# Kernel optimization log

Measured on AMD Instinct MI355X. Metric: run time of the kernel, lower is better.

The kernel has to match this reference:

```python
import jax, jax.numpy as jnp
import numpy as np

REPR_IN = (16, 16, 8)
REPR_OUT = (32, 16, 8)
NUM_BASIS = 16
MAX_RADIUS = 2.0
GAMMA = 16.0  # radial basis sharpness

def _dim(repr_):
    return sum(m * (2 * l + 1) for l, m in enumerate(repr_))

DIM_IN = _dim(REPR_IN)          # 104
SIZE_OUT = _dim(REPR_OUT)       # 120
NUM_GATES = sum(REPR_OUT[1:])   # 24
DIM_OUT = SIZE_OUT + NUM_GATES  # 144 (conv emits gates too)


def setup_inputs() -> dict:
    key = jax.random.key(0)
    k1, k2, k3, k4 = jax.random.split(key, 4)
    B, N, M = 4, 1024, 1024
    features = jax.random.normal(k1, (B, DIM_IN, M), jnp.float32)
    difference_matrix = jax.random.normal(k2, (B, N, M, 3), jnp.float32)
    relative_mask = jax.random.uniform(k3, (B, N, M), jnp.float32)
    W = jax.random.normal(k4, (NUM_BASIS, DIM_OUT, DIM_IN), jnp.float32) / np.sqrt(NUM_BASIS * DIM_IN)
    return {"features": features, "difference_matrix": difference_matrix,
            "relative_mask": relative_mask, "W": W}


def _radial_basis(diff):
    # diff: [B, N, M, 3] -> phi: [B, N, M, K]
    r = jnp.sqrt(jnp.sum(diff * diff, axis=-1) + 1e-12)
    centers = jnp.linspace(0.0, MAX_RADIUS, NUM_BASIS, dtype=diff.dtype)
    return jnp.exp(-GAMMA * jnp.square(r[..., None] - centers))


def reference(features, difference_matrix, relative_mask, W):
    # SE3PointConvolution: per-pair kernel K[b,n,m] = sum_k phi_k(|r_nm|) W[k]
    # masked by relative_mask; out[b,o,n] = sum_m K[b,n,m,o,i] feat[b,i,m].
    # Fused so the [B,N,M,144,104] kernel is never materialized.
    phi = _radial_basis(difference_matrix) * relative_mask[..., None]  # [B,N,M,K]
    tmp = jnp.einsum('bnmk,bim->bnki', phi, features)                  # [B,N,K,DIM_IN]
    y = jnp.einsum('bnki,koi->bon', tmp, W)                            # [B,DIM_OUT,N]

    B, _, N = y.shape
    # scalar (l=0) activation, bias=False
    outs = [jax.nn.relu(y[:, :REPR_OUT[0]])]
    # gates: last NUM_GATES channels, sigmoid
    g = jax.nn.sigmoid(y[:, SIZE_OUT:])
    begin_y, begin_g = REPR_OUT[0], 0
    for l, mul in enumerate(REPR_OUT):
        if l == 0 or mul == 0:
            continue
        d = 2 * l + 1
        fy = y[:, begin_y:begin_y + mul * d].reshape(B, mul, d, N)
        fg = g[:, begin_g:begin_g + mul].reshape(B, mul, 1, N)
        outs.append((fy * fg).reshape(B, mul * d, N))
        begin_y += mul * d
        begin_g += mul
    return jnp.concatenate(outs, axis=1)  # [B, SIZE_OUT, N]
```

## Files before the change

kernel.cpp:

```cpp
#include <hip/hip_runtime.h>


typedef __attribute__((ext_vector_type(4))) float f32x4;
typedef __attribute__((ext_vector_type(8))) short s16x8;

#define DI 104
#define DO 144
#define MT 64
#define PST 72
#define TTST 1688
#define YST 9

#define W_ELEMS 239616
#define F_ELEMS 425984

#define OFF_PHI0 0
#define OFF_PHI1 18432
#define OFF_FEAT0 36864
#define OFF_FEAT1 52992
#define OFF_Y 69120
#define SMEM_TOTAL (69120 + 144*9*4)

__device__ __forceinline__ float fexp2(float x) {
#if __has_builtin(__builtin_amdgcn_exp2f)
    return __builtin_amdgcn_exp2f(x);
#else
    return exp2f(x);
#endif
}
__device__ __forceinline__ float flog2(float x) {
#if __has_builtin(__builtin_amdgcn_logf)
    return __builtin_amdgcn_logf(x);
#else
    return log2f(x);
#endif
}
__device__ __forceinline__ float fsqrt_(float x) {
#if __has_builtin(__builtin_amdgcn_sqrtf)
    return __builtin_amdgcn_sqrtf(x);
#else
    return sqrtf(x);
#endif
}
__device__ __forceinline__ float frcp_(float x) {
#if __has_builtin(__builtin_amdgcn_rcpf)
    return __builtin_amdgcn_rcpf(x);
#else
    return 1.0f / x;
#endif
}
__device__ __forceinline__ unsigned int pkbf(float lo, float hi) {
    unsigned int a = __builtin_bit_cast(unsigned int, lo) + 0x8000u;
    unsigned int b = __builtin_bit_cast(unsigned int, hi) + 0x8000u;
    return __builtin_amdgcn_perm(b, a, 0x07060302u);
}
__device__ __forceinline__ unsigned short f2b(float f) {
    return (unsigned short)((__builtin_bit_cast(unsigned int, f) + 0x8000u) >> 16);
}

__global__ __launch_bounds__(256, 8)
void cvt_kernel(const float* __restrict__ feat_g, const float* __restrict__ W_g,
                unsigned short* __restrict__ ws)
{
    int gid = blockIdx.x * 256 + threadIdx.x;
    const float* src;
    unsigned short* dst;
    if (gid < W_ELEMS/8) {
        src = W_g + gid*8;  dst = ws + gid*8;
    } else {
        int g2 = gid - W_ELEMS/8;
        src = feat_g + g2*8; dst = ws + W_ELEMS + g2*8;
    }
    f32x4 a = *(const f32x4*)src;
    f32x4 b = *(const f32x4*)(src + 4);
    unsigned int o[4] = { pkbf(a[0],a[1]), pkbf(a[2],a[3]), pkbf(b[0],b[1]), pkbf(b[2],b[3]) };
    *(f32x4*)dst = *(f32x4*)o;
}

__global__ __launch_bounds__(512, 4)
void pgb_kernel(const unsigned short* __restrict__ ws,
                const float* __restrict__ diff_g,
                const float* __restrict__ mask_g,
                float* __restrict__ out_g)
{
    const unsigned short* Wbf    = ws;
    const unsigned short* featbf = ws + W_ELEMS;

    __shared__ __align__(16) unsigned char smem[SMEM_TOTAL];
    unsigned short* Tt   = (unsigned short*)(smem);
    float*          ylds = (float*)(smem + OFF_Y);

    const int t    = threadIdx.x;
    const int b    = blockIdx.x >> 7;
    const int n0   = (blockIdx.x & 127) << 3;
    const int wave = t >> 6;
    const int lane = t & 63;
    const int l15  = lane & 15;
    const int q    = lane >> 4;
    const int wr   = wave >> 1;
    const int ct0  = (wave & 1) << 2;

    {
        unsigned int* p0 = (unsigned int*)(smem + OFF_FEAT0 + DI*PST*2);
        unsigned int* p1 = (unsigned int*)(smem + OFF_FEAT1 + DI*PST*2);
        if (t < 288) { p0[t] = 0u; p1[t] = 0u; }
    }

    f32x4 acc[2][4];
#pragma unroll
    for (int rr = 0; rr < 2; ++rr)
#pragma unroll
        for (int cc = 0; cc < 4; ++cc)
            acc[rr][cc] = (f32x4){0.f, 0.f, 0.f, 0.f};

    const int pn = t >> 6;
    const int kh = (t >> 5) & 1;
    const int pm = (t & 31) << 1;
    const float CEXP = -23.083120654223414f;
    const float A1   = 6.155498841126244f;
    const float V2   = -0.8207331788168325f;
    const float K0OFF = kh ? 1.0666666666666667f : 0.f;
    const float S0B   = kh ? -6.976232019943076f : -0.41036658940841624f;
    const size_t dmrow = (size_t)((b << 10) + n0 + pn) << 10;

    const int fi0 = t >> 3, part0 = (t & 7) << 3;
    const int fi1 = 64 + (t >> 3);
    const size_t fbase = (size_t)b * DI << 10;

    float dx0, dy0, dz0, dx1, dy1, dz1, mk0, mk1;
    s16x8 fr0, fr1;
    {
        const float* dp = diff_g + (dmrow + pm)*3;
        dx0=dp[0]; dy0=dp[1]; dz0=dp[2]; dx1=dp[3]; dy1=dp[4]; dz1=dp[5];
        const float* mp = mask_g + dmrow + pm;
        mk0=mp[0]; mk1=mp[1];
        fr0 = *(const s16x8*)(featbf + fbase + ((size_t)fi0 << 10) + part0);
        if (t < 320)
            fr1 = *(const s16x8*)(featbf + fbase + ((size_t)fi1 << 10) + part0);
    }

    for (int s = 0; s < 16; ++s) {
        const int ms = s * MT;
        unsigned short* phibuf  = (unsigned short*)(smem + ((s & 1) ? OFF_PHI1 : OFF_PHI0));
        unsigned short* featbuf = (unsigned short*)(smem + ((s & 1) ? OFF_FEAT1 : OFF_FEAT0));
        float nx0=0, ny0=0, nz0=0, nx1=0, ny1=0, nz1=0, nm0=0, nm1=0;
        s16x8 nf0, nf1;
        if (s < 15) {
            const float* dp = diff_g + (dmrow + ms + MT + pm)*3;
            nx0=dp[0]; ny0=dp[1]; nz0=dp[2]; nx1=dp[3]; ny1=dp[4]; nz1=dp[5];
            const float* mp = mask_g + dmrow + ms + MT + pm;
            nm0=mp[0]; nm1=mp[1];
            nf0 = *(const s16x8*)(featbf + fbase + ((size_t)fi0 << 10) + ms + MT + part0);
            if (t < 320)
                nf1 = *(const s16x8*)(featbf + fbase + ((size_t)fi1 << 10) + ms + MT + part0);
        }
        {
            float r0 = fsqrt_(fmaf(dx0,dx0, fmaf(dy0,dy0, fmaf(dz0,dz0, 1e-12f))));
            float r1 = fsqrt_(fmaf(dx1,dx1, fmaf(dy1,dy1, fmaf(dz1,dz1, 1e-12f))));
            float t0 = r0 - K0OFF, t1 = r1 - K0OFF;
            float E0 = fmaf(CEXP*t0, t0, flog2(mk0));
            float E1 = fmaf(CEXP*t1, t1, flog2(mk1));
            float s0 = fmaf(A1, r0, S0B);
            float s1 = fmaf(A1, r1, S0B);
            unsigned short* pw = phibuf + (pn*16 + kh*8)*PST + pm;
#pragma unroll
            for (int j = 0; j < 8; ++j) {
                float p0 = fexp2(E0);
                float p1 = fexp2(E1);
                *(unsigned int*)(pw + j*PST) = pkbf(p0, p1);
                E0 += s0; s0 += V2;
                E1 += s1; s1 += V2;
            }
        }
        *(s16x8*)(featbuf + fi0*PST + part0) = fr0;
        if (t < 320)
            *(s16x8*)(featbuf + fi1*PST + part0) = fr1;
        __syncthreads();
#pragma unroll
        for (int kk = 0; kk < 2; ++kk) {
            const int mo = kk*32 + q*8;
            s16x8 a0 = *(const s16x8*)(phibuf + ((2*wr    )*16 + l15)*PST + mo);
            s16x8 a1 = *(const s16x8*)(phibuf + ((2*wr + 1)*16 + l15)*PST + mo);
#pragma unroll
            for (int cc = 0; cc < 4; ++cc) {
                if (ct0 + cc < 7) {
                    s16x8 bf = *(const s16x8*)(featbuf + ((ct0+cc)*16 + l15)*PST + mo);
                    acc[0][cc] = __builtin_amdgcn_mfma_f32_16x16x32_bf16(a0, bf, acc[0][cc], 0, 0, 0);
                    acc[1][cc] = __builtin_amdgcn_mfma_f32_16x16x32_bf16(a1, bf, acc[1][cc], 0, 0, 0);
                }
            }
        }
        dx0=nx0; dy0=ny0; dz0=nz0; dx1=nx1; dy1=ny1; dz1=nz1; mk0=nm0; mk1=nm1;
        fr0 = nf0; if (t < 320) fr1 = nf1;
    }

    __syncthreads();

#pragma unroll
    for (int rr = 0; rr < 2; ++rr) {
        int nloc = 2*wr + rr;
#pragma unroll
        for (int cc = 0; cc < 4; ++cc) {
            int i = (ct0+cc)*16 + l15;
            if (ct0 + cc < 7 && i < DI) {
#pragma unroll
                for (int r = 0; r < 4; ++r)
                    Tt[nloc*TTST + (q*4+r)*DI + i] = f2b(acc[rr][cc][r]);
            }
        }
    }
    __syncthreads();

    f32x4 y0 = (f32x4){0.f,0.f,0.f,0.f}, y1 = (f32x4){0.f,0.f,0.f,0.f};
    const int o0 = wave*16 + l15;
    const int o1 = 128 + l15;
#pragma unroll 4
    for (int s3 = 0; s3 < 52; ++s3) {
        int a = s3*4 + q;
        int k = a / 13;
        int i = (a - k*13) << 3;
        s16x8 bf = *(const s16x8*)(Tt + (l15 & 7)*TTST + s3*32 + q*8);
        s16x8 af = *(const s16x8*)(Wbf + (size_t)(k*DO + o0)*DI + i);
        y0 = __builtin_amdgcn_mfma_f32_16x16x32_bf16(af, bf, y0, 0, 0, 0);
        if (wave == 0) {
            s16x8 ag = *(const s16x8*)(Wbf + (size_t)(k*DO + o1)*DI + i);
            y1 = __builtin_amdgcn_mfma_f32_16x16x32_bf16(ag, bf, y1, 0, 0, 0);
        }
    }
    if (l15 < 8) {
#pragma unroll
        for (int r = 0; r < 4; ++r)
            ylds[(wave*16 + q*4 + r)*YST + l15] = y0[r];
        if (wave == 0) {
#pragma unroll
            for (int r = 0; r < 4; ++r)
                ylds[(128 + q*4 + r)*YST + l15] = y1[r];
        }
    }
    __syncthreads();

    const float L2E = 1.4426950408889634f;
    for (int idx = t; idx < 120*8; idx += 512) {
        int o = idx >> 3, nn = idx & 7;
        float y = ylds[o*YST + nn];
        float v;
        if (o < 32) {
            v = fmaxf(y, 0.f);
        } else if (o < 80) {
            float g = ylds[(120 + (o-32)/3)*YST + nn];
            v = y * frcp_(1.f + fexp2(-g*L2E));
        } else {
            float g = ylds[(136 + (o-80)/5)*YST + nn];
            v = y * frcp_(1.f + fexp2(-g*L2E));
        }
        out_g[((size_t)(b*120 + o) << 10) + n0 + nn] = v;
    }
}

extern "C" void kernel_launch(void* const* d_in, const int* in_sizes, int n_in,
                              void* d_out, int out_size, void* d_ws, size_t ws_size,
                              hipStream_t stream) {
    const float* feat = (const float*)d_in[0];
    const float* diff = (const float*)d_in[1];
    const float* mask = (const float*)d_in[2];
    const float* W    = (const float*)d_in[3];
    float* out = (float*)d_out;
    unsigned short* ws = (unsigned short*)d_ws;
    (void)in_sizes; (void)n_in; (void)out_size; (void)ws_size;
    cvt_kernel<<<dim3((W_ELEMS + F_ELEMS)/8/256), dim3(256), 0, stream>>>(feat, W, ws);
    pgb_kernel<<<dim3(512), dim3(512), 0, stream>>>(ws, diff, mask, out);
}
```

Baseline: 142.4 us.

## Swizzle LDS tiles instead of padding and move next-tile prefetch after barrier

The padded LDS row stride (72) for the phi and feature tiles is replaced by an unpadded 64-element stride with an XOR swizzle on 8-element chunks, applied on both the write and the MFMA operand read paths. This shrinks shared memory use while still avoiding bank conflicts. Global loads for the next tile now go after the barrier straight into the live registers, which drops the separate next-tile registers and can lower register pressure. The risk is that load latency is less hidden behind the phi computation.

```diff
diff --git a/kernel.cpp b/kernel.cpp
--- a/kernel.cpp
+++ b/kernel.cpp
@@ -7,7 +7,6 @@
 #define DI 104
 #define DO 144
 #define MT 64
-#define PST 72
 #define TTST 1688
 #define YST 9
 
@@ -15,11 +14,11 @@
 #define F_ELEMS 425984
 
 #define OFF_PHI0 0
-#define OFF_PHI1 18432
-#define OFF_FEAT0 36864
-#define OFF_FEAT1 52992
-#define OFF_Y 69120
-#define SMEM_TOTAL (69120 + 144*9*4)
+#define OFF_PHI1 16384
+#define OFF_FEAT0 32768
+#define OFF_FEAT1 47104
+#define OFF_Y 61440
+#define SMEM_TOTAL (61440 + 144*9*4)
 
 __device__ __forceinline__ float fexp2(float x) {
 #if __has_builtin(__builtin_amdgcn_exp2f)
@@ -99,11 +98,11 @@
     const int q    = lane >> 4;
     const int wr   = wave >> 1;
     const int ct0  = (wave & 1) << 2;
-
-    {
-        unsigned int* p0 = (unsigned int*)(smem + OFF_FEAT0 + DI*PST*2);
-        unsigned int* p1 = (unsigned int*)(smem + OFF_FEAT1 + DI*PST*2);
-        if (t < 288) { p0[t] = 0u; p1[t] = 0u; }
+    const int sw   = l15 & 7;
+
+    if (t < 256) {
+        ((unsigned int*)(smem + OFF_FEAT0 + DI*128))[t] = 0u;
+        ((unsigned int*)(smem + OFF_FEAT1 + DI*128))[t] = 0u;
     }
 
     f32x4 acc[2][4];
@@ -115,7 +114,9 @@
 
     const int pn = t >> 6;
     const int kh = (t >> 5) & 1;
-    const int pm = (t & 31) << 1;
+    const int pml = (t & 31) << 1;
+    const int pblk = (t & 31) >> 2;
+    const int pin  = pml & 7;
     const float CEXP = -23.083120654223414f;
     const float A1   = 6.155498841126244f;
     const float V2   = -0.8207331788168325f;
@@ -123,37 +124,27 @@
     const float S0B   = kh ? -6.976232019943076f : -0.41036658940841624f;
     const size_t dmrow = (size_t)((b << 10) + n0 + pn) << 10;
 
-    const int fi0 = t >> 3, part0 = (t & 7) << 3;
+    const int fi0 = t >> 3, fj = t & 7;
     const int fi1 = 64 + (t >> 3);
+    const int fjs = (fj ^ (fi0 & 7)) << 3;
     const size_t fbase = (size_t)b * DI << 10;
 
     float dx0, dy0, dz0, dx1, dy1, dz1, mk0, mk1;
-    s16x8 fr0, fr1;
+    s16x8 fr0 = {}, fr1 = {};
     {
-        const float* dp = diff_g + (dmrow + pm)*3;
+        const float* dp = diff_g + (dmrow + pml)*3;
         dx0=dp[0]; dy0=dp[1]; dz0=dp[2]; dx1=dp[3]; dy1=dp[4]; dz1=dp[5];
-        const float* mp = mask_g + dmrow + pm;
+        const float* mp = mask_g + dmrow + pml;
         mk0=mp[0]; mk1=mp[1];
-        fr0 = *(const s16x8*)(featbf + fbase + ((size_t)fi0 << 10) + part0);
+        fr0 = *(const s16x8*)(featbf + fbase + ((size_t)fi0 << 10) + (fj << 3));
         if (t < 320)
-            fr1 = *(const s16x8*)(featbf + fbase + ((size_t)fi1 << 10) + part0);
+            fr1 = *(const s16x8*)(featbf + fbase + ((size_t)fi1 << 10) + (fj << 3));
     }
 
     for (int s = 0; s < 16; ++s) {
         const int ms = s * MT;
         unsigned short* phibuf  = (unsigned short*)(smem + ((s & 1) ? OFF_PHI1 : OFF_PHI0));
         unsigned short* featbuf = (unsigned short*)(smem + ((s & 1) ? OFF_FEAT1 : OFF_FEAT0));
-        float nx0=0, ny0=0, nz0=0, nx1=0, ny1=0, nz1=0, nm0=0, nm1=0;
-        s16x8 nf0, nf1;
-        if (s < 15) {
-            const float* dp = diff_g + (dmrow + ms + MT + pm)*3;
-            nx0=dp[0]; ny0=dp[1]; nz0=dp[2]; nx1=dp[3]; ny1=dp[4]; nz1=dp[5];
-            const float* mp = mask_g + dmrow + ms + MT + pm;
-            nm0=mp[0]; nm1=mp[1];
-            nf0 = *(const s16x8*)(featbf + fbase + ((size_t)fi0 << 10) + ms + MT + part0);
-            if (t < 320)
-                nf1 = *(const s16x8*)(featbf + fbase + ((size_t)fi1 << 10) + ms + MT + part0);
-        }
         {
             float r0 = fsqrt_(fmaf(dx0,dx0, fmaf(dy0,dy0, fmaf(dz0,dz0, 1e-12f))));
             float r1 = fsqrt_(fmaf(dx1,dx1, fmaf(dy1,dy1, fmaf(dz1,dz1, 1e-12f))));
@@ -162,36 +153,43 @@
             float E1 = fmaf(CEXP*t1, t1, flog2(mk1));
             float s0 = fmaf(A1, r0, S0B);
             float s1 = fmaf(A1, r1, S0B);
-            unsigned short* pw = phibuf + (pn*16 + kh*8)*PST + pm;
+            unsigned short* pw = phibuf + (pn*16 + kh*8)*64 + pin;
 #pragma unroll
             for (int j = 0; j < 8; ++j) {
                 float p0 = fexp2(E0);
                 float p1 = fexp2(E1);
-                *(unsigned int*)(pw + j*PST) = pkbf(p0, p1);
+                *(unsigned int*)(pw + j*64 + ((pblk ^ j) << 3)) = pkbf(p0, p1);
                 E0 += s0; s0 += V2;
                 E1 += s1; s1 += V2;
             }
         }
-        *(s16x8*)(featbuf + fi0*PST + part0) = fr0;
+        *(s16x8*)(featbuf + fi0*64 + fjs) = fr0;
         if (t < 320)
-            *(s16x8*)(featbuf + fi1*PST + part0) = fr1;
+            *(s16x8*)(featbuf + fi1*64 + fjs) = fr1;
         __syncthreads();
+        if (s < 15) {
+            const float* dp = diff_g + (dmrow + ms + MT + pml)*3;
+            dx0=dp[0]; dy0=dp[1]; dz0=dp[2]; dx1=dp[3]; dy1=dp[4]; dz1=dp[5];
+            const float* mp = mask_g + dmrow + ms + MT + pml;
+            mk0=mp[0]; mk1=mp[1];
+            fr0 = *(const s16x8*)(featbf + fbase + ((size_t)fi0 << 10) + ms + MT + (fj << 3));
+            if (t < 320)
+                fr1 = *(const s16x8*)(featbf + fbase + ((size_t)fi1 << 10) + ms + MT + (fj << 3));
+        }
 #pragma unroll
         for (int kk = 0; kk < 2; ++kk) {
-            const int mo = kk*32 + q*8;
-            s16x8 a0 = *(const s16x8*)(phibuf + ((2*wr    )*16 + l15)*PST + mo);
-            s16x8 a1 = *(const s16x8*)(phibuf + ((2*wr + 1)*16 + l15)*PST + mo);
+            const int mo = ((kk*4 + q) ^ sw) << 3;
+            s16x8 a0 = *(const s16x8*)(phibuf + ((2*wr    )*16 + l15)*64 + mo);
+            s16x8 a1 = *(const s16x8*)(phibuf + ((2*wr + 1)*16 + l15)*64 + mo);
 #pragma unroll
             for (int cc = 0; cc < 4; ++cc) {
                 if (ct0 + cc < 7) {
-                    s16x8 bf = *(const s16x8*)(featbuf + ((ct0+cc)*16 + l15)*PST + mo);
+                    s16x8 bf = *(const s16x8*)(featbuf + ((ct0+cc)*16 + l15)*64 + mo);
                     acc[0][cc] = __builtin_amdgcn_mfma_f32_16x16x32_bf16(a0, bf, acc[0][cc], 0, 0, 0);
                     acc[1][cc] = __builtin_amdgcn_mfma_f32_16x16x32_bf16(a1, bf, acc[1][cc], 0, 0, 0);
                 }
             }
         }
-        dx0=nx0; dy0=ny0; dz0=nz0; dx1=nx1; dy1=ny1; dz1=nz1; mk0=nm0; mk1=nm1;
-        fr0 = nf0; if (t < 320) fr1 = nf1;
     }
 
     __syncthreads();
```

Result: no change. 142.5 us (+0.1%).
